# Kernel tuning notes

Measured on AMD Instinct MI355X. Metric: run time of the kernel, lower is better.

Reference implementation:

```python
import math
import jax, jax.numpy as jnp
import numpy as np

B_IN, B_OUT = 16, 16
F_IN, F_OUT, BATCH = 32, 64, 4
N_ALPHA, N_GAMMA = 4, 3
KERNEL_BETA = math.pi / 8.0
L_TOT = sum((2 * l + 1) ** 2 for l in range(B_OUT))  # 5456


def _lg(n):
    return math.lgamma(n + 1.0)


def _small_d(l, beta):
    """Wigner small-d matrix d^l_{m,n}(beta), [2l+1, 2l+1], Condon-Shortley phase."""
    c, s = math.cos(0.5 * beta), math.sin(0.5 * beta)
    d = np.zeros((2 * l + 1, 2 * l + 1), dtype=np.float64)
    for mi, m in enumerate(range(-l, l + 1)):
        for ni, n in enumerate(range(-l, l + 1)):
            pref = 0.5 * (_lg(l + m) + _lg(l - m) + _lg(l + n) + _lg(l - n))
            acc = 0.0
            for k in range(max(0, n - m), min(l + n, l - m) + 1):
                ln = pref - _lg(l + n - k) - _lg(k) - _lg(m - n + k) - _lg(l - m - k)
                acc += ((-1.0) ** (m - n + k)) * math.exp(ln) * (c ** (2 * l + n - m - 2 * k)) * (s ** (m - n + 2 * k))
            d[mi, ni] = acc
    return d


def _qweights(b):
    """Kostelec-Rockmore SOFT quadrature weights over the 2b beta samples."""
    k = np.arange(b)
    w = np.array([
        (2.0 / b) * math.sin(math.pi * (2 * j + 1) / (4.0 * b)) *
        np.sum(np.sin((2 * j + 1) * (2 * k + 1) * math.pi / (4.0 * b)) / (2 * k + 1))
        for j in range(2 * b)])
    return w


def _wigner_table(betas, b_out, scale_fn):
    rows = []
    for beta in betas:
        blocks = [(_small_d(l, beta) * scale_fn(l)).ravel() for l in range(b_out)]
        rows.append(np.concatenate(blocks))
    return np.stack(rows)  # [len(betas), L_TOT]


def _grid_basis(grid, b_out):
    """conj(D^l_{mn}(a,b,g)) = e^{+i m a} d^l_{mn}(b) e^{+i n g}, flattened over (l,m,n)."""
    cols = []
    for (a, bb, g) in grid:
        blocks = []
        for l in range(b_out):
            m = np.arange(-l, l + 1)
            d = _small_d(l, bb)
            ph = np.exp(1j * (m[:, None] * a + m[None, :] * g))
            blocks.append((d * ph).ravel())
        cols.append(np.concatenate(blocks))
    return np.stack(cols, axis=1)  # [L_TOT, n_grid] complex


def _freq_indices(b_out, nfft):
    ms, ns = [], []
    for l in range(b_out):
        r = np.arange(-l, l + 1)
        M, N = np.meshgrid(r, r, indexing='ij')
        ms.append(np.mod(M.ravel(), nfft))
        ns.append(np.mod(N.ravel(), nfft))
    return np.concatenate(ms), np.concatenate(ns)


def make_grid():
    alphas = [2.0 * math.pi * i / N_ALPHA for i in range(N_ALPHA)]
    gammas = [2.0 * math.pi * i / N_GAMMA for i in range(N_GAMMA)]
    return [(a, KERNEL_BETA, g) for a in alphas for g in gammas]


def setup_inputs() -> dict:
    key = jax.random.key(0)
    k1, k2 = jax.random.split(key)
    x = jax.random.normal(k1, (BATCH, F_IN, 2 * B_IN, 2 * B_IN, 2 * B_IN), jnp.float32)
    grid = make_grid()
    n_grid = len(grid)
    stdv = 1.0 / math.sqrt(n_grid * F_IN * (B_OUT ** 3) / float(B_IN ** 3))
    kernel = stdv * jax.random.normal(k2, (F_IN, F_OUT, n_grid), jnp.float32)
    bias = jnp.zeros((1, F_OUT, 1, 1, 1), jnp.float32)
    # analysis table: quadrature weight * d, with (2pi/2b)^2/(8pi^2) = 1/(8 b^2) absorbed
    betas_in = np.pi * (2 * np.arange(2 * B_IN) + 1) / (4.0 * B_IN)
    w = _qweights(B_IN) / (8.0 * B_IN ** 2)
    wig_f = _wigner_table(betas_in, B_OUT, lambda l: 1.0) * w[:, None]
    # synthesis table: (2l+1) * d, times (2b)^2 to cancel ifft2 normalization
    betas_out = np.pi * (2 * np.arange(2 * B_OUT) + 1) / (4.0 * B_OUT)
    wig_i = _wigner_table(betas_out, B_OUT, lambda l: (2 * l + 1) * (2 * B_OUT) ** 2)
    D = _grid_basis(grid, B_OUT)
    return {
        'x': x, 'kernel': kernel, 'bias': bias,
        'wigner_fwd': jnp.asarray(wig_f, jnp.float32),
        'wigner_inv': jnp.asarray(wig_i, jnp.float32),
        'D_re': jnp.asarray(D.real, jnp.float32),
        'D_im': jnp.asarray(D.imag, jnp.float32),
    }


def reference(x, kernel, bias, wigner_fwd, wigner_inv, D_re, D_im):
    batch, fin = x.shape[0], x.shape[1]
    fout = kernel.shape[1]
    midx_in, nidx_in = _freq_indices(B_OUT, 2 * B_IN)
    midx_out, nidx_out = _freq_indices(B_OUT, 2 * B_OUT)
    # --- SO3 FFT of input: FFT over (alpha, gamma), weighted beta-sum with Wigner-d ---
    Xf = jnp.fft.fft2(x.astype(jnp.complex64), axes=(-2, -1))   # [z,i,beta,ma,ng]
    Xg = Xf[..., midx_in, nidx_in]                               # [z,i,beta,L]
    xh = jnp.einsum('bl,zibl->lzi', wigner_fwd.astype(jnp.complex64), Xg)  # [L,z,i]
    # --- local FT of kernel on SO(3) grid points ---
    Dc = jax.lax.complex(D_re, D_im)                             # [L, n_grid]
    yh = jnp.einsum('lj,ioj->lio', Dc, kernel.astype(jnp.complex64))       # [L,i,o]
    # --- per-frequency block matmul (SO3_mm): z^l = x^l @ y^l, contracting f_in ---
    zs, begin = [], 0
    for l in range(B_OUT):
        n = 2 * l + 1
        xl = xh[begin:begin + n * n].reshape(n, n, batch, fin)
        yl = yh[begin:begin + n * n].reshape(n, n, fin, fout)
        zs.append(jnp.einsum('mkzi,knio->mnzo', xl, yl).reshape(n * n, batch, fout))
        begin += n * n
    zh = jnp.concatenate(zs, axis=0)                             # [L,z,o]
    # --- inverse SO3 FFT: scatter (l,m,n) -> FFT bins, ifft over (alpha,gamma) ---
    term = jnp.einsum('bl,lzo->zobl', wigner_inv.astype(jnp.complex64), zh)
    ng = 2 * B_OUT
    Zf = jnp.zeros((batch, fout, ng, ng, ng), jnp.complex64)
    Zf = Zf.at[..., midx_out, nidx_out].add(term)
    out = jnp.fft.ifft2(Zf, axes=(-2, -1)).real.astype(x.dtype)
    return out + bias
```

## Files before the change

kernel.cpp:

```cpp
#include <hip/hip_runtime.h>
#include <math.h>


typedef unsigned short u16;
typedef unsigned int   u32;
typedef __attribute__((ext_vector_type(8))) short  short8;
typedef __attribute__((ext_vector_type(4))) float  floatx4;

constexpr int LTOT = 5456;

constexpr int LB[17] = {0,1,10,35,84,165,286,455,680,969,
                        1330,1771,2300,2925,3654,4495,5456};

__device__ inline u16 f2bf(float f) {
    u32 u = __float_as_uint(f);
    u += 0x7fff + ((u >> 16) & 1);
    return (u16)(u >> 16);
}
__device__ inline u32 pack2bf(float re, float im) {
    return (u32)f2bf(re) | ((u32)f2bf(im) << 16);
}

__device__ inline short8 btr4(uint4 q, u32 sel, u32 msk) {
    uint4 t;
    t.x = __builtin_amdgcn_perm(q.x, q.x, sel) ^ msk;
    t.y = __builtin_amdgcn_perm(q.y, q.y, sel) ^ msk;
    t.z = __builtin_amdgcn_perm(q.z, q.z, sel) ^ msk;
    t.w = __builtin_amdgcn_perm(q.w, q.w, sel) ^ msk;
    return *(short8*)&t;
}

__global__ __launch_bounds__(256) void k_wtr(const float* __restrict__ w,
                                             float* __restrict__ wT) {
    int t  = blockIdx.x * 256 + threadIdx.x;
    int bq = blockIdx.y;
    if (t < LTOT) {
        float4 v;
        v.x = w[(size_t)(bq * 4 + 0) * LTOT + t];
        v.y = w[(size_t)(bq * 4 + 1) * LTOT + t];
        v.z = w[(size_t)(bq * 4 + 2) * LTOT + t];
        v.w = w[(size_t)(bq * 4 + 3) * LTOT + t];
        *(float4*)(wT + ((size_t)bq * LTOT + t) * 4) = v;
    }
}

__global__ __launch_bounds__(512) void k_fft_fwd(const float* __restrict__ x,
                                                 u32* __restrict__ Xfb) {
    __shared__ float xs[1056];
    __shared__ float Gre[1056], Gim[1056];
    __shared__ float Wc[32], Ws[32];
    int tid = threadIdx.x;
    if (tid < 32) {
        float sv, cv;
        sincosf(6.28318530717958647692f * (float)tid / 32.0f, &sv, &cv);
        Wc[tid] = cv; Ws[tid] = sv;
    }
    const float* src = x + (size_t)blockIdx.x * 1024;
    for (int e = tid; e < 1024; e += 512) xs[(e >> 5) * 33 + (e & 31)] = src[e];
    __syncthreads();
    {
        int a = tid >> 4, k = tid & 15;
        const float* row = &xs[a * 33];
        float Er = 0.f, Ei = 0.f, Or = 0.f, Oi = 0.f;
#pragma unroll
        for (int h = 0; h < 16; h++) {
            int idx = (2 * h * k) & 31;
            float c = Wc[idx], s = Ws[idx];
            float xe = row[2 * h], xo = row[2 * h + 1];
            Er += xe * c;  Ei -= xe * s;
            Or += xo * c;  Oi -= xo * s;
        }
        float WOr = Or * Wc[k] + Oi * Ws[k];
        float WOi = Oi * Wc[k] - Or * Ws[k];
        Gre[a * 33 + k]      = Er + WOr;
        Gim[a * 33 + k]      = Ei + WOi;
        Gre[a * 33 + k + 16] = Er - WOr;
        Gim[a * 33 + k + 16] = Ei - WOi;
    }
    __syncthreads();
    {
        u32* dst = Xfb + (size_t)blockIdx.x * 512;
        int ng = tid & 31, ma = tid >> 5;
        float Er = 0.f, Ei = 0.f, Or = 0.f, Oi = 0.f;
#pragma unroll
        for (int h = 0; h < 16; h++) {
            int idx = (2 * h * ma) & 31;
            float c = Wc[idx], s = Ws[idx];
            float er = Gre[(2 * h) * 33 + ng],      ei = Gim[(2 * h) * 33 + ng];
            float orr = Gre[(2 * h + 1) * 33 + ng], oi = Gim[(2 * h + 1) * 33 + ng];
            Er += er * c + ei * s;   Ei += ei * c - er * s;
            Or += orr * c + oi * s;  Oi += oi * c - orr * s;
        }
        float WOr = Or * Wc[ma] + Oi * Ws[ma];
        float WOi = Oi * Wc[ma] - Or * Ws[ma];
        dst[ma * 32 + ng] = pack2bf(Er + WOr, Ei + WOi);
    }
}

__global__ __launch_bounds__(256) void k_prep_B(const float* __restrict__ Dre,
                                                const float* __restrict__ Dim,
                                                const float* __restrict__ ker,
                                                u32* __restrict__ yhb) {
    __shared__ float Ds[8][24];
    int t0  = blockIdx.x * 8;
    int tid = threadIdx.x;
    if (tid < 192) {
        int rr = tid / 24, jj = tid - rr * 24;
        Ds[rr][jj] = (jj < 12) ? Dre[(t0 + rr) * 12 + jj] : Dim[(t0 + rr) * 12 + jj - 12];
    }
    __syncthreads();
    for (int rep = 0; rep < 8; rep++) {
        int io = rep * 256 + tid;
        int i  = io >> 6, o = io & 63;
        int nio = ((i >> 4) << 10) + ((o >> 5) << 9) + (((o >> 3) & 3) << 7)
                + (((i >> 2) & 3) << 5) + ((o & 7) << 2) + (i & 3);
        const float4* kp = (const float4*)(ker + io * 12);
        float4 ka = kp[0], kb = kp[1], kc = kp[2];
        float kv[12] = {ka.x, ka.y, ka.z, ka.w, kb.x, kb.y, kb.z, kb.w,
                        kc.x, kc.y, kc.z, kc.w};
#pragma unroll
        for (int rr = 0; rr < 8; rr++) {
            float sr = 0.f, si = 0.f;
#pragma unroll
            for (int j = 0; j < 12; j++) {
                sr += Ds[rr][j]      * kv[j];
                si += Ds[rr][12 + j] * kv[j];
            }
            yhb[(size_t)(t0 + rr) * 2048 + nio] = pack2bf(sr, si);
        }
    }
}

__global__ __launch_bounds__(256) void k_beta_A(const u32* __restrict__ Xfb,
                                                const float* __restrict__ wfT,
                                                u16* __restrict__ Ab) {
    int ma  = blockIdx.x >> 6;
    int zig = blockIdx.x & 63;
    int tid = threadIdx.x;
    int ng  = tid & 31;
    int lq  = (tid >> 5) & 3;
    int zil = tid >> 7;
    int zi  = zig * 2 + zil;
    int z = zi >> 5, i = zi & 31;
    int mh = (ma <= 15) ? ma : ma - 32;
    int nh = (ng <= 15) ? ng : ng - 32;
    int am = mh < 0 ? -mh : mh;
    int an = nh < 0 ? -nh : nh;
    int l0 = am > an ? am : an;
    int lb = lq * 4;

    int isconj = (ma > 16);
    int mau = isconj ? (32 - ma) : ma;
    int ngu = isconj ? ((32 - ng) & 31) : ng;
    if (mau > 15) { mau = 0; ngu = 0; }

    int tl[4];
#pragma unroll
    for (int j = 0; j < 4; j++) {
        int l = lb + j;
        tl[j] = LB[l] + (mh + l) * (2 * l + 1) + (nh + l);
    }
    float2 acc[4];
#pragma unroll
    for (int j = 0; j < 4; j++) acc[j] = make_float2(0.f, 0.f);

    const u32* xp = Xfb + (size_t)zi * 32 * 512 + mau * 32 + ngu;
    float sgn = isconj ? -1.f : 1.f;
#pragma unroll 2
    for (int bq = 0; bq < 8; bq++) {
        u32 p0 = xp[(size_t)(4 * bq + 0) * 512];
        u32 p1 = xp[(size_t)(4 * bq + 1) * 512];
        u32 p2 = xp[(size_t)(4 * bq + 2) * 512];
        u32 p3 = xp[(size_t)(4 * bq + 3) * 512];
        float vx0 = __uint_as_float(p0 << 16);
        float vy0 = sgn * __uint_as_float(p0 & 0xffff0000u);
        float vx1 = __uint_as_float(p1 << 16);
        float vy1 = sgn * __uint_as_float(p1 & 0xffff0000u);
        float vx2 = __uint_as_float(p2 << 16);
        float vy2 = sgn * __uint_as_float(p2 & 0xffff0000u);
        float vx3 = __uint_as_float(p3 << 16);
        float vy3 = sgn * __uint_as_float(p3 & 0xffff0000u);
        const float4* wq = (const float4*)(wfT + (size_t)bq * (LTOT * 4));
#pragma unroll
        for (int j = 0; j < 4; j++) {
            if (lb + j >= l0) {
                float4 w = wq[tl[j]];
                acc[j].x += w.x * vx0 + w.y * vx1 + w.z * vx2 + w.w * vx3;
                acc[j].y += w.x * vy0 + w.y * vy1 + w.z * vy2 + w.w * vy3;
            }
        }
    }
    int s_i  = i >> 4;
    int kl   = 2 * (i & 15);
    int joff = kl & 7;
    int Lhi  = (kl >> 3) << 4;
#pragma unroll
    for (int j = 0; j < 4; j++) {
        int l = lb + j;
        if (l >= l0) {
            int mi = mh + l, ni = nh + l;
            int s   = 2 * ni + s_i;
            int row = 4 * mi + z;
            u32 pack = pack2bf(acc[j].x, acc[j].y);
            size_t off = (size_t)8192 * l * l + (size_t)s * 4096
                       + ((row >> 4) << 9) + ((Lhi + (row & 15)) << 3) + joff;
            *(u32*)(Ab + off) = pack;
        }
    }
}

__global__ __launch_bounds__(256) void k_gemm(const u16* __restrict__ Ab,
                                              const u32* __restrict__ yhb,
                                              float* __restrict__ zhT) {
    int rem = blockIdx.x, l, nl = 1;
    for (l = 15; l >= 0; l--) {
        nl = 2 * l + 1;
        int c = nl * 4;
        if (rem < c) break;
        rem -= c;
    }
    int n  = rem >> 2;
    int oq = rem & 3;
    int base = LB[l];
    const u16* Ag = Ab + (size_t)8192 * l * l;
    int S = 2 * nl;

    int tid = threadIdx.x, lane = tid & 63, w = tid >> 6;
    int cc = lane & 1;
    u32 sel = cc ? 0x01000302u : 0x03020100u;
    u32 msk = cc ? 0u          : 0x80000000u;

    const u32* Bb = yhb + (size_t)(base + n) * 2048 + (oq << 8) + ((lane >> 1) << 2);
    const u16* Aw = Ag + ((w << 10) | (lane << 3));

    floatx4 acc[2][2];
#pragma unroll
    for (int a = 0; a < 2; a++)
#pragma unroll
        for (int b = 0; b < 2; b++) acc[a][b] = (floatx4)0.f;

#define LOADB(s, q0, q1) { \
    const uint4* bp = (const uint4*)(Bb + (size_t)((s) >> 1) * nl * 2048 + (((s) & 1) << 10)); \
    q0 = bp[0]; q1 = bp[32]; }
#define LOADA(s, r0, r1) { \
    const u16* apx = Aw + (size_t)(s) * 4096; \
    r0 = *(const short8*)apx; r1 = *(const short8*)(apx + 512); }
#define MF(a, b, c) __builtin_amdgcn_mfma_f32_16x16x32_bf16(a, b, c, 0, 0, 0)

    uint4 eB0, eB1; short8 ea0, ea1;
    uint4 oB0, oB1; short8 oa0, oa1;
    LOADA(0, ea0, ea1); LOADB(0, eB0, eB1);
    LOADA(1, oa0, oa1); LOADB(1, oB0, oB1);

    for (int s = 0; s < S; s += 2) {
        short8 bf0 = btr4(eB0, sel, msk), bf1 = btr4(eB1, sel, msk);
        short8 af0 = ea0, af1 = ea1;
        LOADA(s + 2, ea0, ea1); LOADB(s + 2, eB0, eB1);
        acc[0][0] = MF(af0, bf0, acc[0][0]);  acc[1][0] = MF(af1, bf0, acc[1][0]);
        acc[0][1] = MF(af0, bf1, acc[0][1]);  acc[1][1] = MF(af1, bf1, acc[1][1]);
        short8 cf0 = btr4(oB0, sel, msk), cf1 = btr4(oB1, sel, msk);
        short8 ag0 = oa0, ag1 = oa1;
        LOADA(s + 3, oa0, oa1); LOADB(s + 3, oB0, oB1);
        acc[0][0] = MF(ag0, cf0, acc[0][0]);  acc[1][0] = MF(ag1, cf0, acc[1][0]);
        acc[0][1] = MF(ag0, cf1, acc[0][1]);  acc[1][1] = MF(ag1, cf1, acc[1][1]);
    }
#undef LOADB
#undef LOADA
#undef MF

    int q = lane >> 4, cn = lane & 15;
#pragma unroll
    for (int mt = 0; mt < 2; mt++) {
#pragma unroll
        for (int nt = 0; nt < 2; nt++) {
            int nu2 = (nt << 4) + cn;
            int o2  = (oq << 4) + (nu2 >> 1);
            int c2  = nu2 & 1;
#pragma unroll
            for (int r = 0; r < 4; r++) {
                int R = (w << 5) + (mt << 4) + (q << 2) + r;
                int m = R >> 2, z = R & 3;
                if (m < nl) {
                    int t  = base + m * nl + n;
                    int zo = (z << 6) + o2;
                    zhT[((size_t)zo * LTOT + t) * 2 + c2] = acc[mt][nt][r];
                }
            }
        }
    }
}

__global__ __launch_bounds__(256, 8) void k_inv2(const float2* __restrict__ zhT,
                                                 const float* __restrict__ wiT,
                                                 const float* __restrict__ bias,
                                                 float* __restrict__ out) {
    __shared__ float2 Pb[4 * 528];
    __shared__ float Wc[32], Ws[32];
    int tid = threadIdx.x;
    int zo = blockIdx.x & 255;
    int bq = blockIdx.x >> 8;
    int b0 = bq * 4;
    if (tid < 32) {
        float sv, cv;
        sincosf(6.28318530717958647692f * (float)tid / 32.0f, &sv, &cv);
        Wc[tid] = cv; Ws[tid] = sv;
    }
    {
        int ng = tid & 31, rq = tid >> 5;
        int nh = (ng <= 15) ? ng : ng - 32;
        int an = nh < 0 ? -nh : nh;
        const float2* zr = zhT + (size_t)zo * LTOT;
        const float4* wp = (const float4*)(wiT + (size_t)bq * (LTOT * 4));
#pragma unroll
        for (int mr = 0; mr < 2; mr++) {
            int ma = rq + 8 * mr;
            int l0 = ma > an ? ma : an;
            float2 a0 = make_float2(0.f, 0.f), a1 = a0, a2 = a0, a3 = a0;
#pragma unroll 4
            for (int l = 0; l < 16; l++) {
                if (l >= l0) {
                    int t = LB[l] + (ma + l) * (2 * l + 1) + (nh + l);
                    float2 zv = zr[t];
                    float4 w = wp[t];
                    a0.x += w.x * zv.x; a0.y += w.x * zv.y;
                    a1.x += w.y * zv.x; a1.y += w.y * zv.y;
                    a2.x += w.z * zv.x; a2.y += w.z * zv.y;
                    a3.x += w.w * zv.x; a3.y += w.w * zv.y;
                }
            }
            int po = ma * 33 + ng;
            Pb[po]            = a0;
            Pb[528 + po]      = a1;
            Pb[2 * 528 + po]  = a2;
            Pb[3 * 528 + po]  = a3;
        }
    }
    __syncthreads();
#pragma unroll
    for (int it = 0; it < 2; it++) {
        int task = tid + it * 256;
        int rowid = task >> 3, q = task & 7;
        float2* prow = &Pb[(rowid >> 4) * 528 + (rowid & 15) * 33];
        float2 E0 = make_float2(0.f, 0.f), O0 = E0, E1 = E0, O1 = E0;
        int k1 = q + 8;
#pragma unroll 4
        for (int h = 0; h < 16; h++) {
            float2 e = prow[2 * h], o = prow[2 * h + 1];
            int i0 = (2 * h * q) & 31;
            int i1 = (2 * h * k1) & 31;
            float c0 = Wc[i0], s0 = Ws[i0];
            float c1 = Wc[i1], s1 = Ws[i1];
            E0.x += e.x * c0 - e.y * s0;  E0.y += e.x * s0 + e.y * c0;
            O0.x += o.x * c0 - o.y * s0;  O0.y += o.x * s0 + o.y * c0;
            E1.x += e.x * c1 - e.y * s1;  E1.y += e.x * s1 + e.y * c1;
            O1.x += o.x * c1 - o.y * s1;  O1.y += o.x * s1 + o.y * c1;
        }
        float c0 = Wc[q],  s0 = Ws[q];
        float c1 = Wc[k1], s1 = Ws[k1];
        float2 w0 = make_float2(O0.x * c0 - O0.y * s0, O0.x * s0 + O0.y * c0);
        float2 w1 = make_float2(O1.x * c1 - O1.y * s1, O1.x * s1 + O1.y * c1);
        prow[q]      = make_float2(E0.x + w0.x, E0.y + w0.y);
        prow[q + 16] = make_float2(E0.x - w0.x, E0.y - w0.y);
        prow[q + 8]  = make_float2(E1.x + w1.x, E1.y + w1.y);
        prow[q + 24] = make_float2(E1.x - w1.x, E1.y - w1.y);
    }
    __syncthreads();
    float bv = bias[zo & 63];
#pragma unroll
    for (int it = 0; it < 2; it++) {
        int task = tid + it * 256;
        int p = task >> 7, rr = task & 127;
        int qa = rr >> 5, g = rr & 31;
        const float2* pc = &Pb[p * 528];
        float2 c0 = pc[g];
        float Ea[4], Oa[4];
#pragma unroll
        for (int jj = 0; jj < 4; jj++) { Ea[jj] = c0.x; Oa[jj] = 0.f; }
#pragma unroll 4
        for (int j = 1; j < 8; j++) {
            float2 c = pc[(2 * j) * 33 + g];
#pragma unroll
            for (int jj = 0; jj < 4; jj++) {
                int a = qa * 4 + jj;
                int idx = ((2 * j) * a) & 31;
                Ea[jj] += 2.f * (c.x * Wc[idx] - c.y * Ws[idx]);
            }
        }
#pragma unroll 4
        for (int j = 0; j < 8; j++) {
            float2 c = pc[(2 * j + 1) * 33 + g];
#pragma unroll
            for (int jj = 0; jj < 4; jj++) {
                int a = qa * 4 + jj;
                int idx = ((2 * j + 1) * a) & 31;
                Oa[jj] += 2.f * (c.x * Wc[idx] - c.y * Ws[idx]);
            }
        }
        float* dst = out + (size_t)zo * 32768 + (size_t)(b0 + p) * 1024;
#pragma unroll
        for (int jj = 0; jj < 4; jj++) {
            int a = qa * 4 + jj;
            dst[a * 32 + g]        = (Ea[jj] + Oa[jj]) * (1.f / 1024.f) + bv;
            dst[(a + 16) * 32 + g] = (Ea[jj] - Oa[jj]) * (1.f / 1024.f) + bv;
        }
    }
}

extern "C" void kernel_launch(void* const* d_in, const int* in_sizes, int n_in,
                              void* d_out, int out_size, void* d_ws, size_t ws_size,
                              hipStream_t stream) {
    const float* x    = (const float*)d_in[0];
    const float* ker  = (const float*)d_in[1];
    const float* bias = (const float*)d_in[2];
    const float* wf   = (const float*)d_in[3];
    const float* wi   = (const float*)d_in[4];
    const float* Dre  = (const float*)d_in[5];
    const float* Dim  = (const float*)d_in[6];
    float* out = (float*)d_out;

    char* ws = (char*)d_ws;
    u32*    yhb = (u32*)ws;
    u16*    Ab  = (u16*)(ws + 44695552);
    float*  zhT = (float*)(ws + 44695552 + 4194304);
    u32*    Xfb = (u32*)zhT;
    float*  wfT = (float*)(ws + 44695552 + 4194304 + 8388608);
    float*  wiT = (float*)ws;

    hipLaunchKernelGGL(k_fft_fwd, dim3(4096),  dim3(512), 0, stream, x, Xfb);
    hipLaunchKernelGGL(k_wtr,     dim3(22, 8), dim3(256), 0, stream, wf, wfT);
    hipLaunchKernelGGL(k_prep_B,  dim3(682),   dim3(256), 0, stream, Dre, Dim, ker, yhb);
    hipLaunchKernelGGL(k_beta_A,  dim3(2048),  dim3(256), 0, stream, Xfb, wfT, Ab);
    hipLaunchKernelGGL(k_gemm,    dim3(1024),  dim3(256), 0, stream, Ab, yhb, zhT);
    hipLaunchKernelGGL(k_wtr,     dim3(22, 8), dim3(256), 0, stream, wi, wiT);
    hipLaunchKernelGGL(k_inv2,    dim3(2048),  dim3(256), 0, stream,
                       (const float2*)zhT, wiT, bias, out);
}
```

Baseline: 221.3 us.

## Rewrite inverse DFT stages with packed-FP32 complex math and twiddle recurrences

Rewrites the k_inv2 inverse FFT stages so twiddle factors come from complex recurrences (t *= r) instead of per-iteration shared-memory sin/cos lookups. It also uses v_pk_fma_f32 inline asm for complex multiply-accumulate and for the Wigner weight accumulation, and splits the sums into even/odd parity terms so one pass produces two output bins. LDS row padding changes to 34 with 16-byte vector loads. The recurrences may add small rounding drift, and the inline asm ties the code to CDNA packed-math encoding.

```diff
diff --git a/kernel.cpp b/kernel.cpp
--- a/kernel.cpp
+++ b/kernel.cpp
@@ -6,6 +6,7 @@
 typedef unsigned int   u32;
 typedef __attribute__((ext_vector_type(8))) short  short8;
 typedef __attribute__((ext_vector_type(4))) float  floatx4;
+typedef __attribute__((ext_vector_type(2))) float  f32x2;
 
 constexpr int LTOT = 5456;
 
@@ -28,6 +29,30 @@
     t.z = __builtin_amdgcn_perm(q.z, q.z, sel) ^ msk;
     t.w = __builtin_amdgcn_perm(q.w, q.w, sel) ^ msk;
     return *(short8*)&t;
+}
+
+__device__ __forceinline__ f32x2 cfma(f32x2 e, f32x2 t, f32x2 acc) {
+    asm("v_pk_fma_f32 %0, %1, %2, %0 op_sel:[0,0,0] op_sel_hi:[0,1,1]\n\t"
+        "v_pk_fma_f32 %0, %1, %2, %0 op_sel:[1,1,0] op_sel_hi:[1,0,1] neg_lo:[0,1,0]"
+        : "+v"(acc) : "v"(e), "v"(t));
+    return acc;
+}
+__device__ __forceinline__ f32x2 cmulp(f32x2 t, f32x2 r) {
+    f32x2 d;
+    asm("v_pk_mul_f32 %0, %1, %2 op_sel:[0,0] op_sel_hi:[0,1]\n\t"
+        "v_pk_fma_f32 %0, %1, %2, %0 op_sel:[1,1,0] op_sel_hi:[1,0,1] neg_lo:[0,1,0]"
+        : "=&v"(d) : "v"(t), "v"(r));
+    return d;
+}
+__device__ __forceinline__ f32x2 fma_bl(f32x2 w2, f32x2 v, f32x2 acc) {
+    asm("v_pk_fma_f32 %0, %1, %2, %0 op_sel:[0,0,0] op_sel_hi:[0,1,1]"
+        : "+v"(acc) : "v"(w2), "v"(v));
+    return acc;
+}
+__device__ __forceinline__ f32x2 fma_bh(f32x2 w2, f32x2 v, f32x2 acc) {
+    asm("v_pk_fma_f32 %0, %1, %2, %0 op_sel:[1,0,0] op_sel_hi:[1,1,1]"
+        : "+v"(acc) : "v"(w2), "v"(v));
+    return acc;
 }
 
 __global__ __launch_bounds__(256) void k_wtr(const float* __restrict__ w,
@@ -294,8 +319,8 @@
                                                  const float* __restrict__ wiT,
                                                  const float* __restrict__ bias,
                                                  float* __restrict__ out) {
-    __shared__ float2 Pb[4 * 528];
-    __shared__ float Wc[32], Ws[32];
+    __shared__ __align__(16) f32x2 Pb[4 * 544];
+    __shared__ f32x2 Wf[32];
     int tid = threadIdx.x;
     int zo = blockIdx.x & 255;
     int bq = blockIdx.x >> 8;
@@ -303,36 +328,37 @@
     if (tid < 32) {
         float sv, cv;
         sincosf(6.28318530717958647692f * (float)tid / 32.0f, &sv, &cv);
-        Wc[tid] = cv; Ws[tid] = sv;
+        f32x2 wv; wv.x = cv; wv.y = sv;
+        Wf[tid] = wv;
     }
     {
         int ng = tid & 31, rq = tid >> 5;
         int nh = (ng <= 15) ? ng : ng - 32;
         int an = nh < 0 ? -nh : nh;
-        const float2* zr = zhT + (size_t)zo * LTOT;
-        const float4* wp = (const float4*)(wiT + (size_t)bq * (LTOT * 4));
+        const f32x2* zr = (const f32x2*)zhT + (size_t)zo * LTOT;
+        const f32x2* wp = (const f32x2*)wiT + (size_t)bq * (LTOT * 2);
 #pragma unroll
         for (int mr = 0; mr < 2; mr++) {
             int ma = rq + 8 * mr;
             int l0 = ma > an ? ma : an;
-            float2 a0 = make_float2(0.f, 0.f), a1 = a0, a2 = a0, a3 = a0;
+            f32x2 a0 = (f32x2)0.f, a1 = a0, a2 = a0, a3 = a0;
 #pragma unroll 4
             for (int l = 0; l < 16; l++) {
                 if (l >= l0) {
                     int t = LB[l] + (ma + l) * (2 * l + 1) + (nh + l);
-                    float2 zv = zr[t];
-                    float4 w = wp[t];
-                    a0.x += w.x * zv.x; a0.y += w.x * zv.y;
-                    a1.x += w.y * zv.x; a1.y += w.y * zv.y;
-                    a2.x += w.z * zv.x; a2.y += w.z * zv.y;
-                    a3.x += w.w * zv.x; a3.y += w.w * zv.y;
+                    f32x2 zv = zr[t];
+                    f32x2 w01 = wp[2 * t], w23 = wp[2 * t + 1];
+                    a0 = fma_bl(w01, zv, a0);
+                    a1 = fma_bh(w01, zv, a1);
+                    a2 = fma_bl(w23, zv, a2);
+                    a3 = fma_bh(w23, zv, a3);
                 }
             }
-            int po = ma * 33 + ng;
+            int po = ma * 34 + ng;
             Pb[po]            = a0;
-            Pb[528 + po]      = a1;
-            Pb[2 * 528 + po]  = a2;
-            Pb[3 * 528 + po]  = a3;
+            Pb[544 + po]      = a1;
+            Pb[2 * 544 + po]  = a2;
+            Pb[3 * 544 + po]  = a3;
         }
     }
     __syncthreads();
@@ -340,69 +366,70 @@
     for (int it = 0; it < 2; it++) {
         int task = tid + it * 256;
         int rowid = task >> 3, q = task & 7;
-        float2* prow = &Pb[(rowid >> 4) * 528 + (rowid & 15) * 33];
-        float2 E0 = make_float2(0.f, 0.f), O0 = E0, E1 = E0, O1 = E0;
-        int k1 = q + 8;
-#pragma unroll 4
-        for (int h = 0; h < 16; h++) {
-            float2 e = prow[2 * h], o = prow[2 * h + 1];
-            int i0 = (2 * h * q) & 31;
-            int i1 = (2 * h * k1) & 31;
-            float c0 = Wc[i0], s0 = Ws[i0];
-            float c1 = Wc[i1], s1 = Ws[i1];
-            E0.x += e.x * c0 - e.y * s0;  E0.y += e.x * s0 + e.y * c0;
-            O0.x += o.x * c0 - o.y * s0;  O0.y += o.x * s0 + o.y * c0;
-            E1.x += e.x * c1 - e.y * s1;  E1.y += e.x * s1 + e.y * c1;
-            O1.x += o.x * c1 - o.y * s1;  O1.y += o.x * s1 + o.y * c1;
-        }
-        float c0 = Wc[q],  s0 = Ws[q];
-        float c1 = Wc[k1], s1 = Ws[k1];
-        float2 w0 = make_float2(O0.x * c0 - O0.y * s0, O0.x * s0 + O0.y * c0);
-        float2 w1 = make_float2(O1.x * c1 - O1.y * s1, O1.x * s1 + O1.y * c1);
-        prow[q]      = make_float2(E0.x + w0.x, E0.y + w0.y);
-        prow[q + 16] = make_float2(E0.x - w0.x, E0.y - w0.y);
-        prow[q + 8]  = make_float2(E1.x + w1.x, E1.y + w1.y);
-        prow[q + 24] = make_float2(E1.x - w1.x, E1.y - w1.y);
+        f32x2* prow = &Pb[(rowid >> 4) * 544 + (rowid & 15) * 34];
+        const floatx4* prow4 = (const floatx4*)prow;
+        floatx4 eo0 = prow4[0];
+        f32x2 Ep; Ep.x = eo0.x; Ep.y = eo0.y;
+        f32x2 Op; Op.x = eo0.z; Op.y = eo0.w;
+        f32x2 En = (f32x2)0.f, On = (f32x2)0.f;
+        f32x2 r = Wf[2 * q];
+        f32x2 t = r;
+#pragma unroll
+        for (int h = 1; h < 16; h++) {
+            floatx4 eo = prow4[h];
+            f32x2 e; e.x = eo.x; e.y = eo.y;
+            f32x2 o; o.x = eo.z; o.y = eo.w;
+            if (h & 1) { En = cfma(e, t, En); On = cfma(o, t, On); }
+            else       { Ep = cfma(e, t, Ep); Op = cfma(o, t, Op); }
+            if (h < 15) t = cmulp(t, r);
+        }
+        f32x2 E0 = Ep + En, E1 = Ep - En;
+        f32x2 O0 = Op + On, O1 = Op - On;
+        f32x2 wq = Wf[q];
+        f32x2 w0 = cmulp(O0, wq);
+        f32x2 u1 = cmulp(O1, wq);
+        f32x2 w1; w1.x = -u1.y; w1.y = u1.x;
+        prow[q]      = E0 + w0;
+        prow[q + 16] = E0 - w0;
+        prow[q + 8]  = E1 + w1;
+        prow[q + 24] = E1 - w1;
     }
     __syncthreads();
     float bv = bias[zo & 63];
 #pragma unroll
-    for (int it = 0; it < 2; it++) {
+    for (int it = 0; it < 4; it++) {
         int task = tid + it * 256;
-        int p = task >> 7, rr = task & 127;
+        int p = task >> 8, rr = task & 255;
         int qa = rr >> 5, g = rr & 31;
-        const float2* pc = &Pb[p * 528];
-        float2 c0 = pc[g];
-        float Ea[4], Oa[4];
-#pragma unroll
-        for (int jj = 0; jj < 4; jj++) { Ea[jj] = c0.x; Oa[jj] = 0.f; }
-#pragma unroll 4
+        const f32x2* pc = &Pb[p * 544];
+        f32x2 r = Wf[2 * qa];
+        f32x2 u = Wf[qa];
+        f32x2 Uee = (f32x2)0.f, Ueo = Uee, Ve = Uee, Vo = Uee;
+        f32x2 c0 = pc[g];
+        {
+            f32x2 c1 = pc[34 + g];
+            Ve = cfma(c1, u, Ve);
+        }
+        f32x2 t = r;
+        u = cmulp(u, r);
+#pragma unroll
         for (int j = 1; j < 8; j++) {
-            float2 c = pc[(2 * j) * 33 + g];
-#pragma unroll
-            for (int jj = 0; jj < 4; jj++) {
-                int a = qa * 4 + jj;
-                int idx = ((2 * j) * a) & 31;
-                Ea[jj] += 2.f * (c.x * Wc[idx] - c.y * Ws[idx]);
-            }
-        }
-#pragma unroll 4
-        for (int j = 0; j < 8; j++) {
-            float2 c = pc[(2 * j + 1) * 33 + g];
-#pragma unroll
-            for (int jj = 0; jj < 4; jj++) {
-                int a = qa * 4 + jj;
-                int idx = ((2 * j + 1) * a) & 31;
-                Oa[jj] += 2.f * (c.x * Wc[idx] - c.y * Ws[idx]);
-            }
-        }
+            f32x2 ce = pc[(2 * j) * 34 + g];
+            f32x2 co = pc[(2 * j + 1) * 34 + g];
+            if (j & 1) { Ueo = cfma(ce, t, Ueo); Vo = cfma(co, u, Vo); }
+            else       { Uee = cfma(ce, t, Uee); Ve = cfma(co, u, Ve); }
+            if (j < 7) { t = cmulp(t, r); u = cmulp(u, r); }
+        }
+        float EaA = c0.x + 2.f * (Uee.x + Ueo.x);
+        float EaB = c0.x + 2.f * (Uee.x - Ueo.x);
+        float OaA = 2.f * (Ve.x + Vo.x);
+        float OaB = -2.f * (Ve.y - Vo.y);
         float* dst = out + (size_t)zo * 32768 + (size_t)(b0 + p) * 1024;
-#pragma unroll
-        for (int jj = 0; jj < 4; jj++) {
-            int a = qa * 4 + jj;
-            dst[a * 32 + g]        = (Ea[jj] + Oa[jj]) * (1.f / 1024.f) + bv;
-            dst[(a + 16) * 32 + g] = (Ea[jj] - Oa[jj]) * (1.f / 1024.f) + bv;
-        }
+        constexpr float sc = 1.f / 1024.f;
+        dst[qa * 32 + g]         = (EaA + OaA) * sc + bv;
+        dst[(qa + 16) * 32 + g]  = (EaA - OaA) * sc + bv;
+        dst[(qa + 8) * 32 + g]   = (EaB + OaB) * sc + bv;
+        dst[(qa + 24) * 32 + g]  = (EaB - OaB) * sc + bv;
     }
 }
 
```

New measurement: 201.3 us. -9.1%, faster.
